# Kernel optimization log

Measured on AMD Instinct MI355X. Metric: run time of the kernel, lower is better.

The kernel has to match this reference:

```python
import jax, jax.numpy as jnp
import numpy as np

N_REF, PHRASE_LEN, ASCII = 50000, 32, 128
BATCH = 16


def setup_inputs() -> dict:
    key = jax.random.key(0)
    k1, k2 = jax.random.split(key)
    x = jax.random.normal(k1, (BATCH, PHRASE_LEN, ASCII), dtype=jnp.float32)
    raw_phrases = jax.random.normal(k2, (N_REF, PHRASE_LEN, ASCII), dtype=jnp.float32)
    return {"x": x, "raw_phrases": raw_phrases}


def reference(x, raw_phrases):
    # dist[b, n] = sum_{l,a} (raw_phrases[n,l,a] - x[b,l,a])**2
    # Expanded form avoids materializing the [B, N, L, A] difference tensor
    # (which would be ~13 GB); exact same math up to fp reassociation.
    r2 = jnp.sum(raw_phrases * raw_phrases, axis=(1, 2))          # [N]
    x2 = jnp.sum(x * x, axis=(1, 2))                              # [B]
    xr = jnp.einsum('bla,nla->bn', x, raw_phrases)                # [B, N]
    dist = r2[None, :] - 2.0 * xr + x2[:, None]                   # [B, N]
    # torch F.softmax on a 1-D tensor (no dim) softmaxes over the reference axis.
    # Note: the original applies softmax to the (positive) distances directly.
    return jax.nn.softmax(dist, axis=-1)                          # [B, N]
```

## Files before the change

### kernel.cpp

```cpp
#include <hip/hip_runtime.h>
#include <math.h>

#define N_REF   50000
#define BATCH   16
#define KDIM    4096
#define CHUNK   256
#define NCHUNK  (KDIM / CHUNK)
#define RPB     16
#define RPW     4

typedef float f32x4 __attribute__((ext_vector_type(4)));
typedef __attribute__((address_space(3))) uint32_t lds_u32;
typedef const __attribute__((address_space(1))) uint32_t glb_u32;

__global__ __launch_bounds__(256) void dist_kernel(const float* __restrict__ x,
                                                   const float* __restrict__ raw,
                                                   float* __restrict__ dist)
{
    __shared__ float xs[2][BATCH * CHUNK];
    const int tid  = threadIdx.x;
    const int lane = tid & 63;
    const int wv   = tid >> 6;
    const long n_base = (long)blockIdx.x * RPB + (long)wv * RPW;

    float acc[BATCH][RPW];
    #pragma unroll
    for (int b = 0; b < BATCH; ++b)
        #pragma unroll
        for (int r = 0; r < RPW; ++r) acc[b][r] = 0.f;
    float r2a[RPW] = {0.f, 0.f, 0.f, 0.f};
    f32x4 rv[RPW];

#define STAGE(buf, c) do {                                                      \
        _Pragma("unroll")                                                       \
        for (int i_ = 0; i_ < 4; ++i_) {                                        \
            const int b_ = i_ * 4 + wv;                                         \
            const float* g_ = x + (size_t)b_ * KDIM + (size_t)(c) * CHUNK + lane * 4; \
            const float* l_ = &xs[buf][b_ * CHUNK];                             \
            __builtin_amdgcn_global_load_lds((glb_u32*)g_, (lds_u32*)l_, 16, 0, 0); \
        }                                                                       \
    } while (0)

#define LOADRV(c) do {                                                          \
        _Pragma("unroll")                                                       \
        for (int r_ = 0; r_ < RPW; ++r_)                                        \
            rv[r_] = __builtin_nontemporal_load(                                \
                (const f32x4*)(raw + (size_t)(n_base + r_) * KDIM               \
                                   + (size_t)(c) * CHUNK + lane * 4));          \
    } while (0)

#define COMPUTE(buf) do {                                                       \
        _Pragma("unroll")                                                       \
        for (int r_ = 0; r_ < RPW; ++r_) {                                      \
            r2a[r_] = fmaf(rv[r_].x, rv[r_].x, r2a[r_]);                        \
            r2a[r_] = fmaf(rv[r_].y, rv[r_].y, r2a[r_]);                        \
            r2a[r_] = fmaf(rv[r_].z, rv[r_].z, r2a[r_]);                        \
            r2a[r_] = fmaf(rv[r_].w, rv[r_].w, r2a[r_]);                        \
        }                                                                       \
        _Pragma("unroll")                                                       \
        for (int b_ = 0; b_ < BATCH; ++b_) {                                    \
            const f32x4 xv_ = *(const f32x4*)(&xs[buf][b_ * CHUNK + lane * 4]); \
            _Pragma("unroll")                                                   \
            for (int r_ = 0; r_ < RPW; ++r_) {                                  \
                acc[b_][r_] = fmaf(rv[r_].x, xv_.x, acc[b_][r_]);               \
                acc[b_][r_] = fmaf(rv[r_].y, xv_.y, acc[b_][r_]);               \
                acc[b_][r_] = fmaf(rv[r_].z, xv_.z, acc[b_][r_]);               \
                acc[b_][r_] = fmaf(rv[r_].w, xv_.w, acc[b_][r_]);               \
            }                                                                   \
        }                                                                       \
    } while (0)

    STAGE(0, 0);
    __syncthreads();

    int buf = 0;
    #pragma unroll 1
    for (int c = 0; c < NCHUNK - 1; ++c) {
        LOADRV(c);
        STAGE(buf ^ 1, c + 1);
        COMPUTE(buf);
        __syncthreads();
        buf ^= 1;
    }
    LOADRV(NCHUNK - 1);
    COMPUTE(buf);

    float vals[64];
    #pragma unroll
    for (int b = 0; b < BATCH; ++b)
        #pragma unroll
        for (int r = 0; r < RPW; ++r) vals[b * RPW + r] = acc[b][r];

    #pragma unroll
    for (int k = 0; k < 6; ++k) {
        const int bit = 1 << k;
        const bool hi = (lane & bit) != 0;
        #pragma unroll
        for (int i = 0; i < (64 >> (k + 1)); ++i) {
            const float a  = vals[2 * i];
            const float bb = vals[2 * i + 1];
            const float keep = hi ? bb : a;
            const float send = hi ? a  : bb;
            const float recv = __shfl_xor(send, bit, 64);
            vals[i] = keep + recv;
        }
    }

    #pragma unroll
    for (int r = 0; r < RPW; ++r) {
        #pragma unroll
        for (int k = 0; k < 6; ++k)
            r2a[r] += __shfl_xor(r2a[r], 1 << k, 64);
    }

    const int b_out = lane >> 2;
    const int r_out = lane & 3;
    const float r2v = (r_out == 0) ? r2a[0] : (r_out == 1) ? r2a[1]
                    : (r_out == 2) ? r2a[2] : r2a[3];
    dist[(size_t)b_out * N_REF + (size_t)(n_base + r_out)] = r2v - 2.0f * vals[0];
}

#define SMB   25
#define SMC   2000

__global__ __launch_bounds__(256) void softmax_part(const float* __restrict__ d,
                                                    float2* __restrict__ part)
{
    const int row = blockIdx.y, cb = blockIdx.x;
    const float* p = d + (size_t)row * N_REF + (size_t)cb * SMC;
    const int tid = threadIdx.x;

    float m = -INFINITY, s = 0.f;
    #pragma unroll
    for (int i = 0; i < 2; ++i) {
        const int q = tid + i * 256;
        if (q < SMC / 4) {
            const float4 v = *(const float4*)(p + q * 4);
            const float M = fmaxf(m, fmaxf(fmaxf(v.x, v.y), fmaxf(v.z, v.w)));
            s = s * __expf(m - M) + __expf(v.x - M) + __expf(v.y - M)
                                  + __expf(v.z - M) + __expf(v.w - M);
            m = M;
        }
    }
    #pragma unroll
    for (int k = 1; k < 64; k <<= 1) {
        const float mo = __shfl_xor(m, k, 64);
        const float so = __shfl_xor(s, k, 64);
        const float M  = fmaxf(m, mo);
        s = s * __expf(m - M) + so * __expf(mo - M);
        m = M;
    }
    __shared__ float2 wsum[4];
    const int wv = tid >> 6, lane = tid & 63;
    if (lane == 0) wsum[wv] = make_float2(m, s);
    __syncthreads();
    if (tid == 0) {
        float M = wsum[0].x, S = wsum[0].y;
        #pragma unroll
        for (int i = 1; i < 4; ++i) {
            const float M2 = fmaxf(M, wsum[i].x);
            S = S * __expf(M - M2) + wsum[i].y * __expf(wsum[i].x - M2);
            M = M2;
        }
        part[row * SMB + cb] = make_float2(M, S);
    }
}

__global__ __launch_bounds__(256) void softmax_norm(float* __restrict__ d,
                                                    const float2* __restrict__ part)
{
    const int row = blockIdx.y, cb = blockIdx.x;
    const int tid = threadIdx.x;

    float M = -INFINITY, S = 0.f;
    #pragma unroll
    for (int i = 0; i < SMB; ++i) {
        const float2 ps = part[row * SMB + i];
        const float M2 = fmaxf(M, ps.x);
        S = S * __expf(M - M2) + ps.y * __expf(ps.x - M2);
        M = M2;
    }
    const float Sinv = 1.f / S;

    float* p = d + (size_t)row * N_REF + (size_t)cb * SMC;
    #pragma unroll
    for (int i = 0; i < 2; ++i) {
        const int q = tid + i * 256;
        if (q < SMC / 4) {
            float4 v = *(float4*)(p + q * 4);
            v.x = __expf(v.x - M) * Sinv;
            v.y = __expf(v.y - M) * Sinv;
            v.z = __expf(v.z - M) * Sinv;
            v.w = __expf(v.w - M) * Sinv;
            *(float4*)(p + q * 4) = v;
        }
    }
}

extern "C" void kernel_launch(void* const* d_in, const int* in_sizes, int n_in,
                              void* d_out, int out_size, void* d_ws, size_t ws_size,
                              hipStream_t stream) {
    const float* x   = (const float*)d_in[0];
    const float* raw = (const float*)d_in[1];
    float* out = (float*)d_out;
    float2* part = (float2*)d_ws;

    dist_kernel<<<N_REF / RPB, 256, 0, stream>>>(x, raw, out);
    softmax_part<<<dim3(SMB, BATCH), 256, 0, stream>>>(out, part);
    softmax_norm<<<dim3(SMB, BATCH), 256, 0, stream>>>(out, part);
}
```

Baseline: 183.7 us.

## Widen K chunk to 512 and single-buffer x staging with explicit vmcnt waits

The reduction chunk doubles from 256 to 512, so each iteration loads two float4 per reference row and there are half as many loop iterations and barriers. The double-buffered LDS staging of x becomes a single buffer. Each iteration issues the x-to-LDS loads first, then the raw loads, and uses s_waitcnt vmcnt(8) so that only the LDS stage must finish before the barrier while the raw loads stay in flight. The aim is more outstanding global bytes per wave and less sync overhead in this bandwidth-bound stream. The cost is that x staging no longer overlaps compute, register pressure rises, and correctness relies on in-order vmcnt accounting.

```diff
diff --git a/kernel.cpp b/kernel.cpp
--- a/kernel.cpp
+++ b/kernel.cpp
@@ -4,7 +4,7 @@
 #define N_REF   50000
 #define BATCH   16
 #define KDIM    4096
-#define CHUNK   256
+#define CHUNK   512
 #define NCHUNK  (KDIM / CHUNK)
 #define RPB     16
 #define RPW     4
@@ -17,7 +17,7 @@
                                                    const float* __restrict__ raw,
                                                    float* __restrict__ dist)
 {
-    __shared__ float xs[2][BATCH * CHUNK];
+    __shared__ float xs[BATCH * CHUNK];
     const int tid  = threadIdx.x;
     const int lane = tid & 63;
     const int wv   = tid >> 6;
@@ -29,61 +29,70 @@
         #pragma unroll
         for (int r = 0; r < RPW; ++r) acc[b][r] = 0.f;
     float r2a[RPW] = {0.f, 0.f, 0.f, 0.f};
-    f32x4 rv[RPW];
-
-#define STAGE(buf, c) do {                                                      \
-        _Pragma("unroll")                                                       \
-        for (int i_ = 0; i_ < 4; ++i_) {                                        \
-            const int b_ = i_ * 4 + wv;                                         \
-            const float* g_ = x + (size_t)b_ * KDIM + (size_t)(c) * CHUNK + lane * 4; \
-            const float* l_ = &xs[buf][b_ * CHUNK];                             \
+    f32x4 rv[RPW][2];
+
+#define STAGE(c) do {                                                           \
+        _Pragma("unroll")                                                       \
+        for (int i_ = 0; i_ < 8; ++i_) {                                        \
+            const int s_ = i_ * 4 + wv;                                         \
+            const int b_ = s_ >> 1;                                             \
+            const int h_ = s_ & 1;                                              \
+            const float* g_ = x + (size_t)b_ * KDIM + (size_t)(c) * CHUNK       \
+                                + h_ * 256 + lane * 4;                          \
+            const float* l_ = &xs[s_ * 256];                                    \
             __builtin_amdgcn_global_load_lds((glb_u32*)g_, (lds_u32*)l_, 16, 0, 0); \
         }                                                                       \
     } while (0)
 
 #define LOADRV(c) do {                                                          \
         _Pragma("unroll")                                                       \
+        for (int r_ = 0; r_ < RPW; ++r_) {                                      \
+            const float* p_ = raw + (size_t)(n_base + r_) * KDIM                \
+                                  + (size_t)(c) * CHUNK + lane * 4;             \
+            rv[r_][0] = __builtin_nontemporal_load((const f32x4*)(p_));         \
+            rv[r_][1] = __builtin_nontemporal_load((const f32x4*)(p_ + 256));   \
+        }                                                                       \
+    } while (0)
+
+#define COMPUTE() do {                                                          \
+        _Pragma("unroll")                                                       \
         for (int r_ = 0; r_ < RPW; ++r_)                                        \
-            rv[r_] = __builtin_nontemporal_load(                                \
-                (const f32x4*)(raw + (size_t)(n_base + r_) * KDIM               \
-                                   + (size_t)(c) * CHUNK + lane * 4));          \
-    } while (0)
-
-#define COMPUTE(buf) do {                                                       \
-        _Pragma("unroll")                                                       \
-        for (int r_ = 0; r_ < RPW; ++r_) {                                      \
-            r2a[r_] = fmaf(rv[r_].x, rv[r_].x, r2a[r_]);                        \
-            r2a[r_] = fmaf(rv[r_].y, rv[r_].y, r2a[r_]);                        \
-            r2a[r_] = fmaf(rv[r_].z, rv[r_].z, r2a[r_]);                        \
-            r2a[r_] = fmaf(rv[r_].w, rv[r_].w, r2a[r_]);                        \
-        }                                                                       \
+            _Pragma("unroll")                                                   \
+            for (int h_ = 0; h_ < 2; ++h_) {                                    \
+                r2a[r_] = fmaf(rv[r_][h_].x, rv[r_][h_].x, r2a[r_]);            \
+                r2a[r_] = fmaf(rv[r_][h_].y, rv[r_][h_].y, r2a[r_]);            \
+                r2a[r_] = fmaf(rv[r_][h_].z, rv[r_][h_].z, r2a[r_]);            \
+                r2a[r_] = fmaf(rv[r_][h_].w, rv[r_][h_].w, r2a[r_]);            \
+            }                                                                   \
         _Pragma("unroll")                                                       \
         for (int b_ = 0; b_ < BATCH; ++b_) {                                    \
-            const f32x4 xv_ = *(const f32x4*)(&xs[buf][b_ * CHUNK + lane * 4]); \
+            const f32x4 xv0 = *(const f32x4*)(&xs[b_ * CHUNK + lane * 4]);      \
+            const f32x4 xv1 = *(const f32x4*)(&xs[b_ * CHUNK + 256 + lane * 4]);\
             _Pragma("unroll")                                                   \
             for (int r_ = 0; r_ < RPW; ++r_) {                                  \
-                acc[b_][r_] = fmaf(rv[r_].x, xv_.x, acc[b_][r_]);               \
-                acc[b_][r_] = fmaf(rv[r_].y, xv_.y, acc[b_][r_]);               \
-                acc[b_][r_] = fmaf(rv[r_].z, xv_.z, acc[b_][r_]);               \
-                acc[b_][r_] = fmaf(rv[r_].w, xv_.w, acc[b_][r_]);               \
+                acc[b_][r_] = fmaf(rv[r_][0].x, xv0.x, acc[b_][r_]);            \
+                acc[b_][r_] = fmaf(rv[r_][0].y, xv0.y, acc[b_][r_]);            \
+                acc[b_][r_] = fmaf(rv[r_][0].z, xv0.z, acc[b_][r_]);            \
+                acc[b_][r_] = fmaf(rv[r_][0].w, xv0.w, acc[b_][r_]);            \
+                acc[b_][r_] = fmaf(rv[r_][1].x, xv1.x, acc[b_][r_]);            \
+                acc[b_][r_] = fmaf(rv[r_][1].y, xv1.y, acc[b_][r_]);            \
+                acc[b_][r_] = fmaf(rv[r_][1].z, xv1.z, acc[b_][r_]);            \
+                acc[b_][r_] = fmaf(rv[r_][1].w, xv1.w, acc[b_][r_]);            \
             }                                                                   \
         }                                                                       \
     } while (0)
 
-    STAGE(0, 0);
-    __syncthreads();
-
-    int buf = 0;
     #pragma unroll 1
-    for (int c = 0; c < NCHUNK - 1; ++c) {
+    for (int c = 0; c < NCHUNK; ++c) {
+        __builtin_amdgcn_s_barrier();
+        __builtin_amdgcn_sched_barrier(0);
+        STAGE(c);
         LOADRV(c);
-        STAGE(buf ^ 1, c + 1);
-        COMPUTE(buf);
-        __syncthreads();
-        buf ^= 1;
-    }
-    LOADRV(NCHUNK - 1);
-    COMPUTE(buf);
+        asm volatile("s_waitcnt vmcnt(8)" ::: "memory");
+        __builtin_amdgcn_s_barrier();
+        __builtin_amdgcn_sched_barrier(0);
+        COMPUTE();
+    }
 
     float vals[64];
     #pragma unroll
```

New measurement: 191.6 us. 1.04x slower.

## Fuse per-block softmax max/sum partials into distance kernel epilogue

Applied to the files above, without the earlier changes.

The distance kernel's epilogue now computes per-block online-softmax (max, sum) partials for each batch row and writes them to a workspace. This removes the separate softmax_part pass that re-read the whole distance matrix. A small merge kernel reduces the 3125 partials per row into a global max and inverse sum, and the normalize kernel uses those. The cost is two extra block barriers and a few shuffles in the dist kernel epilogue, plus a serial merge over 3125 entries per row run on only 16 blocks.

```diff
diff --git a/kernel.cpp b/kernel.cpp
--- a/kernel.cpp
+++ b/kernel.cpp
@@ -8,6 +8,8 @@
 #define NCHUNK  (KDIM / CHUNK)
 #define RPB     16
 #define RPW     4
+#define NBLK    (N_REF / RPB)
+#define PSTRIDE 3200
 
 typedef float f32x4 __attribute__((ext_vector_type(4)));
 typedef __attribute__((address_space(3))) uint32_t lds_u32;
@@ -15,7 +17,8 @@
 
 __global__ __launch_bounds__(256) void dist_kernel(const float* __restrict__ x,
                                                    const float* __restrict__ raw,
-                                                   float* __restrict__ dist)
+                                                   float* __restrict__ dist,
+                                                   float2* __restrict__ part)
 {
     __shared__ float xs[2][BATCH * CHUNK];
     const int tid  = threadIdx.x;
@@ -117,72 +120,82 @@
     const int r_out = lane & 3;
     const float r2v = (r_out == 0) ? r2a[0] : (r_out == 1) ? r2a[1]
                     : (r_out == 2) ? r2a[2] : r2a[3];
-    dist[(size_t)b_out * N_REF + (size_t)(n_base + r_out)] = r2v - 2.0f * vals[0];
+    const float d = r2v - 2.0f * vals[0];
+    dist[(size_t)b_out * N_REF + (size_t)(n_base + r_out)] = d;
+
+    float m = d;
+    m = fmaxf(m, __shfl_xor(m, 1, 64));
+    m = fmaxf(m, __shfl_xor(m, 2, 64));
+    float s = __expf(d - m);
+    s += __shfl_xor(s, 1, 64);
+    s += __shfl_xor(s, 2, 64);
+
+    float2* xs_f2 = (float2*)&xs[0][0];
+    __syncthreads();
+    if ((lane & 3) == 0) xs_f2[wv * BATCH + b_out] = make_float2(m, s);
+    __syncthreads();
+    if (tid < BATCH) {
+        float2 p0 = xs_f2[tid];
+        float M = p0.x, S = p0.y;
+        #pragma unroll
+        for (int w = 1; w < 4; ++w) {
+            const float2 pw = xs_f2[w * BATCH + tid];
+            const float M2 = fmaxf(M, pw.x);
+            S = S * __expf(M - M2) + pw.y * __expf(pw.x - M2);
+            M = M2;
+        }
+        part[(size_t)tid * PSTRIDE + blockIdx.x] = make_float2(M, S);
+    }
+}
+
+__global__ __launch_bounds__(256) void softmax_merge(const float2* __restrict__ part,
+                                                     float2* __restrict__ gms)
+{
+    const int b = blockIdx.x;
+    const int tid = threadIdx.x;
+    float M = -INFINITY, S = 0.f;
+    for (int i = tid; i < NBLK; i += 256) {
+        const float2 p = part[(size_t)b * PSTRIDE + i];
+        const float M2 = fmaxf(M, p.x);
+        S = S * __expf(M - M2) + p.y * __expf(p.x - M2);
+        M = M2;
+    }
+    #pragma unroll
+    for (int k = 1; k < 64; k <<= 1) {
+        const float mo = __shfl_xor(M, k, 64);
+        const float so = __shfl_xor(S, k, 64);
+        const float M2 = fmaxf(M, mo);
+        S = S * __expf(M - M2) + so * __expf(mo - M2);
+        M = M2;
+    }
+    __shared__ float2 wsum[4];
+    const int wv = tid >> 6, lane = tid & 63;
+    if (lane == 0) wsum[wv] = make_float2(M, S);
+    __syncthreads();
+    if (tid == 0) {
+        float Mf = wsum[0].x, Sf = wsum[0].y;
+        #pragma unroll
+        for (int i = 1; i < 4; ++i) {
+            const float M2 = fmaxf(Mf, wsum[i].x);
+            Sf = Sf * __expf(Mf - M2) + wsum[i].y * __expf(wsum[i].x - M2);
+            Mf = M2;
+        }
+        gms[b] = make_float2(Mf, 1.f / Sf);
+    }
 }
 
 #define SMB   25
 #define SMC   2000
 
-__global__ __launch_bounds__(256) void softmax_part(const float* __restrict__ d,
-                                                    float2* __restrict__ part)
+__global__ __launch_bounds__(256) void softmax_norm(float* __restrict__ d,
+                                                    const float2* __restrict__ gms)
 {
     const int row = blockIdx.y, cb = blockIdx.x;
-    const float* p = d + (size_t)row * N_REF + (size_t)cb * SMC;
+    const float2 ms = gms[row];
+    const float M = ms.x, Sinv = ms.y;
+
+    float* p = d + (size_t)row * N_REF + (size_t)cb * SMC;
     const int tid = threadIdx.x;
-
-    float m = -INFINITY, s = 0.f;
-    #pragma unroll
-    for (int i = 0; i < 2; ++i) {
-        const int q = tid + i * 256;
-        if (q < SMC / 4) {
-            const float4 v = *(const float4*)(p + q * 4);
-            const float M = fmaxf(m, fmaxf(fmaxf(v.x, v.y), fmaxf(v.z, v.w)));
-            s = s * __expf(m - M) + __expf(v.x - M) + __expf(v.y - M)
-                                  + __expf(v.z - M) + __expf(v.w - M);
-            m = M;
-        }
-    }
-    #pragma unroll
-    for (int k = 1; k < 64; k <<= 1) {
-        const float mo = __shfl_xor(m, k, 64);
-        const float so = __shfl_xor(s, k, 64);
-        const float M  = fmaxf(m, mo);
-        s = s * __expf(m - M) + so * __expf(mo - M);
-        m = M;
-    }
-    __shared__ float2 wsum[4];
-    const int wv = tid >> 6, lane = tid & 63;
-    if (lane == 0) wsum[wv] = make_float2(m, s);
-    __syncthreads();
-    if (tid == 0) {
-        float M = wsum[0].x, S = wsum[0].y;
-        #pragma unroll
-        for (int i = 1; i < 4; ++i) {
-            const float M2 = fmaxf(M, wsum[i].x);
-            S = S * __expf(M - M2) + wsum[i].y * __expf(wsum[i].x - M2);
-            M = M2;
-        }
-        part[row * SMB + cb] = make_float2(M, S);
-    }
-}
-
-__global__ __launch_bounds__(256) void softmax_norm(float* __restrict__ d,
-                                                    const float2* __restrict__ part)
-{
-    const int row = blockIdx.y, cb = blockIdx.x;
-    const int tid = threadIdx.x;
-
-    float M = -INFINITY, S = 0.f;
-    #pragma unroll
-    for (int i = 0; i < SMB; ++i) {
-        const float2 ps = part[row * SMB + i];
-        const float M2 = fmaxf(M, ps.x);
-        S = S * __expf(M - M2) + ps.y * __expf(ps.x - M2);
-        M = M2;
-    }
-    const float Sinv = 1.f / S;
-
-    float* p = d + (size_t)row * N_REF + (size_t)cb * SMC;
     #pragma unroll
     for (int i = 0; i < 2; ++i) {
         const int q = tid + i * 256;
@@ -204,8 +217,9 @@
     const float* raw = (const float*)d_in[1];
     float* out = (float*)d_out;
     float2* part = (float2*)d_ws;
-
-    dist_kernel<<<N_REF / RPB, 256, 0, stream>>>(x, raw, out);
-    softmax_part<<<dim3(SMB, BATCH), 256, 0, stream>>>(out, part);
-    softmax_norm<<<dim3(SMB, BATCH), 256, 0, stream>>>(out, part);
-}
+    float2* gms  = (float2*)((char*)d_ws + (size_t)BATCH * PSTRIDE * sizeof(float2));
+
+    dist_kernel<<<NBLK, 256, 0, stream>>>(x, raw, out, part);
+    softmax_merge<<<BATCH, 256, 0, stream>>>(part, gms);
+    softmax_norm<<<dim3(SMB, BATCH), 256, 0, stream>>>(out, gms);
+}
```

Measured after the change: 185.7 us. Within noise of the previous version (+1.1%).
